# Performance work log

Measured on AMD Instinct MI355X. Metric: run time of the kernel, lower is better.

## Reference

```python
import jax, jax.numpy as jnp
import numpy as np

D_MODEL = 1024
HEADS = 16
D_K = D_MODEL // HEADS
D_FF = 4096
B, S = 2, 2048
EPS = 1e-5


def setup_inputs() -> dict:
    key = jax.random.key(0)
    ks = jax.random.split(key, 16)
    sc_att = 1.0 / np.sqrt(D_MODEL)
    sc_ff1 = 1.0 / np.sqrt(D_MODEL)
    sc_ff2 = 1.0 / np.sqrt(D_FF)
    return {
        "input": jax.random.normal(ks[0], (B, S, D_MODEL), jnp.float32),
        "mask": jnp.ones((B, 1, 1, S), jnp.int32),
        # stacked per-head projections: [H, D_MODEL, D_K]
        "Wq": jax.random.normal(ks[1], (HEADS, D_MODEL, D_K), jnp.float32) * sc_att,
        "bq": jax.random.normal(ks[2], (HEADS, D_K), jnp.float32) * 0.01,
        "Wk": jax.random.normal(ks[3], (HEADS, D_MODEL, D_K), jnp.float32) * sc_att,
        "bk": jax.random.normal(ks[4], (HEADS, D_K), jnp.float32) * 0.01,
        "Wv": jax.random.normal(ks[5], (HEADS, D_MODEL, D_K), jnp.float32) * sc_att,
        "bv": jax.random.normal(ks[6], (HEADS, D_K), jnp.float32) * 0.01,
        "Wo": jax.random.normal(ks[7], (D_MODEL, D_MODEL), jnp.float32) * sc_att,
        "bo": jax.random.normal(ks[8], (D_MODEL,), jnp.float32) * 0.01,
        "ln1_g": jnp.ones((D_MODEL,), jnp.float32),
        "ln1_b": jnp.zeros((D_MODEL,), jnp.float32),
        "ln2_g": jnp.ones((D_MODEL,), jnp.float32),
        "ln2_b": jnp.zeros((D_MODEL,), jnp.float32),
        "W1": jax.random.normal(ks[9], (D_MODEL, D_FF), jnp.float32) * sc_ff1,
        "b1": jax.random.normal(ks[10], (D_FF,), jnp.float32) * 0.01,
        "W2": jax.random.normal(ks[11], (D_FF, D_MODEL), jnp.float32) * sc_ff2,
        "b2": jax.random.normal(ks[12], (D_MODEL,), jnp.float32) * 0.01,
    }


def _layernorm(x, g, b):
    mu = jnp.mean(x, axis=-1, keepdims=True)
    var = jnp.mean(jnp.square(x - mu), axis=-1, keepdims=True)
    return (x - mu) * jax.lax.rsqrt(var + EPS) * g + b


def reference(input, mask, Wq, bq, Wk, bk, Wv, bv, Wo, bo,
              ln1_g, ln1_b, ln2_g, ln2_b, W1, b1, W2, b2):
    x = input
    # per-head projections, stacked: [B,H,S,D_K]
    q = jnp.einsum('bsd,hdk->bhsk', x, Wq) + bq[None, :, None, :]
    k = jnp.einsum('bsd,hdk->bhsk', x, Wk) + bk[None, :, None, :]
    v = jnp.einsum('bsd,hdk->bhsk', x, Wv) + bv[None, :, None, :]
    scores = jnp.einsum('bhqk,bhsk->bhqs', q, k) / np.sqrt(D_K)  # [B,H,S,S]
    scores = jnp.where(mask == 0, jnp.float32(-1e9), scores)
    attn = jax.nn.softmax(scores, axis=-1)
    ctx = jnp.einsum('bhqs,bhsk->bhqk', attn, v)  # [B,H,S,D_K]
    # concat heads along feature dim (head h occupies slice h*D_K:(h+1)*D_K)
    ctx = jnp.transpose(ctx, (0, 2, 1, 3)).reshape(B, S, D_MODEL)
    att_out = ctx @ Wo + bo
    h = _layernorm(x + att_out, ln1_g, ln1_b)
    ff = jax.nn.relu(h @ W1 + b1) @ W2 + b2
    return _layernorm(h + ff, ln2_g, ln2_b)
```

## Files before the change

### kernel.cpp

```cpp
#include <hip/hip_runtime.h>
#include <cstdint>
#include <cstddef>

typedef unsigned short u16;
typedef unsigned int   u32;
typedef unsigned short u16x4 __attribute__((ext_vector_type(4)));
typedef unsigned short u16x8 __attribute__((ext_vector_type(8)));
typedef unsigned int   u32x2 __attribute__((ext_vector_type(2)));
typedef __bf16 bf16x8 __attribute__((ext_vector_type(8)));
typedef float f32x4 __attribute__((ext_vector_type(4)));

#define MFMA16(a, b, c) __builtin_amdgcn_mfma_f32_16x16x32_bf16((a), (b), (c), 0, 0, 0)

__device__ __forceinline__ float bf2f(u16 h) {
  union { unsigned u; float f; } v; v.u = ((unsigned)h) << 16; return v.f;
}
__device__ __forceinline__ u16 f2bf(float f) {
  union { float f; unsigned u; } v; v.f = f;
  unsigned r = v.u + 0x7fffu + ((v.u >> 16) & 1u);
  return (u16)(r >> 16);
}
__device__ __forceinline__ void gll16(const u16* g, u16* l) {
  __builtin_amdgcn_global_load_lds(
      (const __attribute__((address_space(1))) void*)g,
      (__attribute__((address_space(3))) void*)l, 16, 0, 0);
}
__device__ __forceinline__ float fast_exp2(float x) {
#if __has_builtin(__builtin_amdgcn_exp2f)
  return __builtin_amdgcn_exp2f(x);
#else
  return exp2f(x);
#endif
}

__global__ __launch_bounds__(256) void transpose_qkv(
    const float* __restrict__ Wq, const float* __restrict__ Wk,
    const float* __restrict__ Wv, u16* __restrict__ outb) {
  __shared__ u16 tile[32][33];
  const int z = blockIdx.z;
  const int which = z >> 4, h = z & 15;
  const float* in = (which == 0 ? Wq : (which == 1 ? Wk : Wv)) + (size_t)h * 1024 * 64;
  u16* out = outb + ((size_t)which * 1024 + h * 64) * 1024;
  const int tx = threadIdx.x & 31, ty = threadIdx.x >> 5;
  const int r0 = blockIdx.y * 32, c0 = blockIdx.x * 32;
  #pragma unroll
  for (int i = 0; i < 32; i += 8)
    tile[ty + i][tx] = f2bf(in[(size_t)(r0 + ty + i) * 64 + c0 + tx]);
  __syncthreads();
  #pragma unroll
  for (int i = 0; i < 32; i += 8)
    out[(size_t)(c0 + ty + i) * 1024 + r0 + tx] = tile[tx][ty + i];
}

__global__ __launch_bounds__(256) void transpose_w(
    const float* __restrict__ Wo, const float* __restrict__ W1,
    const float* __restrict__ W2, u16* __restrict__ Wo_t,
    u16* __restrict__ W1_t, u16* __restrict__ W2_t) {
  __shared__ u16 tile[32][33];
  const int id = blockIdx.x;
  const float* in; u16* outp; int R, C, cx, ry;
  if (id < 1024)      { in = Wo; outp = Wo_t; R = 1024; C = 1024; cx = id & 31;  ry = id >> 5; }
  else if (id < 5120) { int t = id - 1024; in = W1; outp = W1_t; R = 1024; C = 4096; cx = t & 127; ry = t >> 7; }
  else                { int t = id - 5120; in = W2; outp = W2_t; R = 4096; C = 1024; cx = t & 31;  ry = t >> 5; }
  const int tx = threadIdx.x & 31, ty = threadIdx.x >> 5;
  const int r0 = ry * 32, c0 = cx * 32;
  #pragma unroll
  for (int i = 0; i < 32; i += 8)
    tile[ty + i][tx] = f2bf(in[(size_t)(r0 + ty + i) * C + c0 + tx]);
  __syncthreads();
  #pragma unroll
  for (int i = 0; i < 32; i += 8)
    outp[(size_t)(c0 + ty + i) * R + r0 + tx] = tile[tx][ty + i];
}

__global__ __launch_bounds__(256) void prep_small(
    const float* __restrict__ bq, const float* __restrict__ bk,
    const float* __restrict__ bv, const int* __restrict__ mask,
    float* __restrict__ biasq, float* __restrict__ madd2) {
  int i = blockIdx.x * 256 + threadIdx.x;
  if (i < 3072) {
    biasq[i] = (i < 1024) ? bq[i] : (i < 2048 ? bk[i - 1024] : bv[i - 2048]);
  } else if (i < 7168) {
    int j = i - 3072;
    madd2[j] = mask[j] ? -23.083120f : -1.442695e9f;
  }
}

__global__ __launch_bounds__(256) void cvt_x(
    const float* __restrict__ in, u16* __restrict__ out, int n) {
  int i = (blockIdx.x * 256 + threadIdx.x) * 4;
  if (i >= n) return;
  const float4 v = *(const float4*)&in[i];
  u16x4 o;
  o[0] = f2bf(v.x); o[1] = f2bf(v.y); o[2] = f2bf(v.z); o[3] = f2bf(v.w);
  *(u16x4*)&out[i] = o;
}

template <int MODE>
__global__ __launch_bounds__(256) void gemm_bt(
    const u16* __restrict__ A, const u16* __restrict__ Bt,
    const float* __restrict__ bias, u16* __restrict__ C,
    int M, int N, int K) {
  __shared__ __align__(16) u16 As[2][128 * 32];
  __shared__ __align__(16) u16 Bs[2][128 * 32];
  const int tid = threadIdx.x;
  const int lane = tid & 63;
  const int wave = tid >> 6;
  const int m0 = blockIdx.y * 128;
  const int n0 = blockIdx.x * 128;
  const int wr = (wave >> 1) * 64;
  const int wc = (wave & 1) * 64;
  const int lrow = lane & 15;
  const int quad = lane >> 4;

  const int srow = lane >> 2;
  const int scol = (lane & 3) * 8;
  const u16* gA1 = &A[(size_t)(m0 + wave * 16 + srow) * K + scol];
  const u16* gA2 = &A[(size_t)(m0 + 64 + wave * 16 + srow) * K + scol];
  const u16* gB1 = &Bt[(size_t)(n0 + wave * 16 + srow) * K + scol];
  const u16* gB2 = &Bt[(size_t)(n0 + 64 + wave * 16 + srow) * K + scol];
  const int so1 = (wave * 16) * 32;
  const int so2 = (wave * 16 + 64) * 32;

  f32x4 acc[4][4];
  #pragma unroll
  for (int i = 0; i < 4; ++i)
    #pragma unroll
    for (int j = 0; j < 4; ++j)
      acc[i][j] = (f32x4){0.f, 0.f, 0.f, 0.f};

  for (int k0 = 0; k0 < K; k0 += 64) {
    gll16(gA1 + k0, &As[0][so1]);
    gll16(gA2 + k0, &As[0][so2]);
    gll16(gB1 + k0, &Bs[0][so1]);
    gll16(gB2 + k0, &Bs[0][so2]);
    gll16(gA1 + k0 + 32, &As[1][so1]);
    gll16(gA2 + k0 + 32, &As[1][so2]);
    gll16(gB1 + k0 + 32, &Bs[1][so1]);
    gll16(gB2 + k0 + 32, &Bs[1][so2]);
    __syncthreads();
    #pragma unroll
    for (int kb = 0; kb < 2; ++kb) {
      bf16x8 af[4], bfr[4];
      #pragma unroll
      for (int i = 0; i < 4; ++i) {
        af[i]  = *(const bf16x8*)&As[kb][(wr + i * 16 + lrow) * 32 + quad * 8];
        bfr[i] = *(const bf16x8*)&Bs[kb][(wc + i * 16 + lrow) * 32 + quad * 8];
      }
      #pragma unroll
      for (int fr = 0; fr < 4; ++fr)
        #pragma unroll
        for (int fc = 0; fc < 4; ++fc)
          acc[fr][fc] = MFMA16(af[fr], bfr[fc], acc[fr][fc]);
    }
    __syncthreads();
  }

  #pragma unroll
  for (int fr = 0; fr < 4; ++fr) {
    int rowb = m0 + wr + fr * 16 + quad * 4;
    #pragma unroll
    for (int fc = 0; fc < 4; ++fc) {
      int col = n0 + wc + fc * 16 + lrow;
      float bv = bias[col];
      #pragma unroll
      for (int r = 0; r < 4; ++r) {
        float v = acc[fr][fc][r] + bv;
        if (MODE == 1) v = fmaxf(v, 0.f);
        C[(size_t)(rowb + r) * N + col] = f2bf(v);
      }
    }
  }
}

__global__ __launch_bounds__(256) void gemm_splitk(
    const u16* __restrict__ A, const u16* __restrict__ Bt,
    u16* __restrict__ Cp, int M, int N, int K) {
  __shared__ __align__(16) u16 As[2][128 * 32];
  __shared__ __align__(16) u16 Bs[2][128 * 32];
  const int tid = threadIdx.x;
  const int lane = tid & 63;
  const int wave = tid >> 6;
  const int m0 = blockIdx.y * 128;
  const int n0 = blockIdx.x * 128;
  const int kz = blockIdx.z;
  const int Kh = K >> 1;
  const int kbase = kz * Kh;
  const int wr = (wave >> 1) * 64;
  const int wc = (wave & 1) * 64;
  const int lrow = lane & 15;
  const int quad = lane >> 4;

  const int srow = lane >> 2;
  const int scol = (lane & 3) * 8;
  const u16* gA1 = &A[(size_t)(m0 + wave * 16 + srow) * K + kbase + scol];
  const u16* gA2 = &A[(size_t)(m0 + 64 + wave * 16 + srow) * K + kbase + scol];
  const u16* gB1 = &Bt[(size_t)(n0 + wave * 16 + srow) * K + kbase + scol];
  const u16* gB2 = &Bt[(size_t)(n0 + 64 + wave * 16 + srow) * K + kbase + scol];
  const int so1 = (wave * 16) * 32;
  const int so2 = (wave * 16 + 64) * 32;
  u16* C = Cp + (size_t)kz * M * N;

  f32x4 acc[4][4];
  #pragma unroll
  for (int i = 0; i < 4; ++i)
    #pragma unroll
    for (int j = 0; j < 4; ++j)
      acc[i][j] = (f32x4){0.f, 0.f, 0.f, 0.f};

  for (int k0 = 0; k0 < Kh; k0 += 64) {
    gll16(gA1 + k0, &As[0][so1]);
    gll16(gA2 + k0, &As[0][so2]);
    gll16(gB1 + k0, &Bs[0][so1]);
    gll16(gB2 + k0, &Bs[0][so2]);
    gll16(gA1 + k0 + 32, &As[1][so1]);
    gll16(gA2 + k0 + 32, &As[1][so2]);
    gll16(gB1 + k0 + 32, &Bs[1][so1]);
    gll16(gB2 + k0 + 32, &Bs[1][so2]);
    __syncthreads();
    #pragma unroll
    for (int kb = 0; kb < 2; ++kb) {
      bf16x8 af[4], bfr[4];
      #pragma unroll
      for (int i = 0; i < 4; ++i) {
        af[i]  = *(const bf16x8*)&As[kb][(wr + i * 16 + lrow) * 32 + quad * 8];
        bfr[i] = *(const bf16x8*)&Bs[kb][(wc + i * 16 + lrow) * 32 + quad * 8];
      }
      #pragma unroll
      for (int fr = 0; fr < 4; ++fr)
        #pragma unroll
        for (int fc = 0; fc < 4; ++fc)
          acc[fr][fc] = MFMA16(af[fr], bfr[fc], acc[fr][fc]);
    }
    __syncthreads();
  }

  #pragma unroll
  for (int fr = 0; fr < 4; ++fr) {
    int rowb = m0 + wr + fr * 16 + quad * 4;
    #pragma unroll
    for (int fc = 0; fc < 4; ++fc) {
      int col = n0 + wc + fc * 16 + lrow;
      #pragma unroll
      for (int r = 0; r < 4; ++r)
        C[(size_t)(rowb + r) * N + col] = f2bf(acc[fr][fc][r]);
    }
  }
}

__global__ __launch_bounds__(256) void attn_kernel(
    const u16* __restrict__ xqkv, const float* __restrict__ madd2,
    u16* __restrict__ ctx) {
  __shared__ __align__(16) u16 Ks[64][72];
  __shared__ __align__(16) u16 Vt[64][136];
  __shared__ __align__(16) u16 Ps[4][2][16][72];
  const int tid = threadIdx.x;
  const int lane = tid & 63;
  const int wave = tid >> 6;
  const int lrow = lane & 15;
  const int quad = lane >> 4;
  const int b = blockIdx.z, h = blockIdx.y;
  const int qb = blockIdx.x * 128 + wave * 16;
  const u16* Qp = xqkv + (size_t)b * 2048 * 3072 + h * 64;
  const u16* Kp = Qp + 1024;
  const u16* Vp = Qp + 2048;
  const float S2 = 0.18033688f;

  bf16x8 qa[2][2];
  #pragma unroll
  for (int t = 0; t < 2; ++t) {
    qa[t][0] = *(const bf16x8*)&Qp[(size_t)(qb + t * 64 + lrow) * 3072 + quad * 8];
    qa[t][1] = *(const bf16x8*)&Qp[(size_t)(qb + t * 64 + lrow) * 3072 + 32 + quad * 8];
  }

  f32x4 o[2][4];
  #pragma unroll
  for (int t = 0; t < 2; ++t)
    #pragma unroll
    for (int i = 0; i < 4; ++i) o[t][i] = (f32x4){0.f, 0.f, 0.f, 0.f};
  float rsum[2] = {0.f, 0.f};

  const int ks_row = tid >> 3, ks_col = (tid & 7) * 8;
  const int v_dg = tid >> 4;
  const int v_kp = tid & 15;
  const float* maddb = madd2 + b * 2048;

  u16x8 kreg[2];
  u16x4 va[2], vb[2];
  #pragma unroll
  for (int sh = 0; sh < 2; ++sh) {
    kreg[sh] = *(const u16x8*)&Kp[(size_t)(sh * 32 + ks_row) * 3072 + ks_col];
    va[sh] = *(const u16x4*)&Vp[(size_t)(sh * 32 + 2 * v_kp) * 3072 + v_dg * 4];
    vb[sh] = *(const u16x4*)&Vp[(size_t)(sh * 32 + 2 * v_kp + 1) * 3072 + v_dg * 4];
  }

  for (int s0 = 0; s0 < 2048; s0 += 64) {
    __syncthreads();
    #pragma unroll
    for (int sh = 0; sh < 2; ++sh) {
      *(u16x8*)&Ks[sh * 32 + ks_row][ks_col] = kreg[sh];
      #pragma unroll
      for (int j = 0; j < 4; ++j) {
        u32 pk = ((u32)vb[sh][j] << 16) | (u32)va[sh][j];
        *(u32*)&Vt[v_dg * 4 + j][sh * 32 + 2 * v_kp] = pk;
      }
    }
    __syncthreads();
    if (s0 + 64 < 2048) {
      #pragma unroll
      for (int sh = 0; sh < 2; ++sh) {
        int sb = s0 + 64 + sh * 32;
        kreg[sh] = *(const u16x8*)&Kp[(size_t)(sb + ks_row) * 3072 + ks_col];
        va[sh] = *(const u16x4*)&Vp[(size_t)(sb + 2 * v_kp) * 3072 + v_dg * 4];
        vb[sh] = *(const u16x4*)&Vp[(size_t)(sb + 2 * v_kp + 1) * 3072 + v_dg * 4];
      }
    }

    bf16x8 kf[4][2], vf[4][2];
    #pragma unroll
    for (int kb = 0; kb < 4; ++kb) {
      kf[kb][0] = *(const bf16x8*)&Ks[kb * 16 + lrow][quad * 8];
      kf[kb][1] = *(const bf16x8*)&Ks[kb * 16 + lrow][32 + quad * 8];
    }
    #pragma unroll
    for (int nb = 0; nb < 4; ++nb) {
      vf[nb][0] = *(const bf16x8*)&Vt[nb * 16 + lrow][quad * 8];
      vf[nb][1] = *(const bf16x8*)&Vt[nb * 16 + lrow][32 + quad * 8];
    }

    #pragma unroll
    for (int t = 0; t < 2; ++t) {
      #pragma unroll
      for (int kb = 0; kb < 4; ++kb) {
        f32x4 z = (f32x4){0.f, 0.f, 0.f, 0.f};
        z = MFMA16(kf[kb][0], qa[t][0], z);
        z = MFMA16(kf[kb][1], qa[t][1], z);
        f32x4 m4 = *(const f32x4*)&maddb[s0 + kb * 16 + quad * 4];
        u32 pb[4];
        #pragma unroll
        for (int r = 0; r < 4; ++r) {
          float p = fast_exp2(fmaf(z[r], S2, m4[r]));
          rsum[t] += p;
          union { float f; u32 u; } cv; cv.f = p;
          pb[r] = cv.u + 0x8000u;
        }
        u32x2 w2;
        w2[0] = __builtin_amdgcn_perm(pb[1], pb[0], 0x07060302);
        w2[1] = __builtin_amdgcn_perm(pb[3], pb[2], 0x07060302);
        *(u32x2*)&Ps[wave][t][lrow][kb * 16 + quad * 4] = w2;
      }
      #pragma unroll
      for (int kh = 0; kh < 2; ++kh) {
        bf16x8 pa = *(const bf16x8*)&Ps[wave][t][lrow][kh * 32 + quad * 8];
        #pragma unroll
        for (int nb = 0; nb < 4; ++nb)
          o[t][nb] = MFMA16(pa, vf[nb][kh], o[t][nb]);
      }
    }
  }

  #pragma unroll
  for (int t = 0; t < 2; ++t) {
    float rs = rsum[t];
    rs += __shfl_xor(rs, 16, 64);
    rs += __shfl_xor(rs, 32, 64);
    float inv = 1.f / fmaxf(rs, 1e-30f);
    #pragma unroll
    for (int r = 0; r < 4; ++r) {
      float invq = __shfl(inv, quad * 4 + r, 64);
      int q = qb + t * 64 + quad * 4 + r;
      #pragma unroll
      for (int nb = 0; nb < 4; ++nb) {
        float v = o[t][nb][r] * invq;
        ctx[((size_t)b * 2048 + q) * 1024 + h * 64 + nb * 16 + lrow] = f2bf(v);
      }
    }
  }
}

template <int IN_BF, int OUT_BF>
__global__ __launch_bounds__(256) void add_ln2p(
    const void* __restrict__ xa_, const u16* __restrict__ p0,
    const u16* __restrict__ p1, const float* __restrict__ cb,
    const float* __restrict__ g, const float* __restrict__ bb,
    void* __restrict__ outp_) {
  __shared__ float red[8];
  const int tid = threadIdx.x;
  const size_t base = (size_t)blockIdx.x * 1024;
  const float* xf = (const float*)xa_;
  const u16*   xb = (const u16*)xa_;
  float v[4];
  float s = 0.f;
  #pragma unroll
  for (int i = 0; i < 4; ++i) {
    int c = i * 256 + tid;
    float xv = IN_BF ? bf2f(xb[base + c]) : xf[base + c];
    v[i] = xv + bf2f(p0[base + c]) + bf2f(p1[base + c]) + cb[c];
    s += v[i];
  }
  #pragma unroll
  for (int off = 32; off > 0; off >>= 1) s += __shfl_down(s, off, 64);
  if ((tid & 63) == 0) red[tid >> 6] = s;
  __syncthreads();
  float mean = (red[0] + red[1] + red[2] + red[3]) * (1.f / 1024.f);
  float s2 = 0.f;
  #pragma unroll
  for (int i = 0; i < 4; ++i) { float d = v[i] - mean; s2 += d * d; }
  #pragma unroll
  for (int off = 32; off > 0; off >>= 1) s2 += __shfl_down(s2, off, 64);
  if ((tid & 63) == 0) red[4 + (tid >> 6)] = s2;
  __syncthreads();
  float var = (red[4] + red[5] + red[6] + red[7]) * (1.f / 1024.f);
  float rstd = rsqrtf(var + 1e-5f);
  #pragma unroll
  for (int i = 0; i < 4; ++i) {
    int c = i * 256 + tid;
    float r = (v[i] - mean) * rstd * g[c] + bb[c];
    if (OUT_BF) ((u16*)outp_)[base + c] = f2bf(r);
    else        ((float*)outp_)[base + c] = r;
  }
}

extern "C" void kernel_launch(void* const* d_in, const int* in_sizes, int n_in,
                              void* d_out, int out_size, void* d_ws, size_t ws_size,
                              hipStream_t stream) {
  (void)in_sizes; (void)n_in; (void)out_size; (void)ws_size;
  const float* x    = (const float*)d_in[0];
  const int*   mask = (const int*)d_in[1];
  const float* Wq   = (const float*)d_in[2];
  const float* bq   = (const float*)d_in[3];
  const float* Wk   = (const float*)d_in[4];
  const float* bk   = (const float*)d_in[5];
  const float* Wv   = (const float*)d_in[6];
  const float* bv   = (const float*)d_in[7];
  const float* Wo   = (const float*)d_in[8];
  const float* bo   = (const float*)d_in[9];
  const float* ln1g = (const float*)d_in[10];
  const float* ln1b = (const float*)d_in[11];
  const float* ln2g = (const float*)d_in[12];
  const float* ln2b = (const float*)d_in[13];
  const float* W1   = (const float*)d_in[14];
  const float* b1   = (const float*)d_in[15];
  const float* W2   = (const float*)d_in[16];
  const float* b2   = (const float*)d_in[17];
  float* out = (float*)d_out;

  char* ws = (char*)d_ws;
  u16*   Wqkv_t = (u16*)(ws + 0);
  u16*   fp     = (u16*)(ws + 0);
  u16*   Wo_t   = (u16*)(ws + 6291456);
  u16*   W1_t   = (u16*)(ws + 8388608);
  u16*   W2_t   = (u16*)(ws + 16777216);
  u16*   xqkv   = (u16*)(ws + 25165824);
  u16*   wp     = (u16*)(ws + 25165824);
  u16*   xb     = (u16*)(ws + 50331648);
  u16*   ctx    = (u16*)(ws + 50331648);
  u16*   ff1    = (u16*)(ws + 25165824);
  u16*   hbuf   = (u16*)(ws + 67108864);
  float* biasq  = (float*)(ws + 75497472);
  float* madd2  = (float*)(ws + 75509760);

  prep_small<<<28, 256, 0, stream>>>(bq, bk, bv, mask, biasq, madd2);
  transpose_qkv<<<dim3(2, 32, 48), 256, 0, stream>>>(Wq, Wk, Wv, Wqkv_t);
  transpose_w<<<9216, 256, 0, stream>>>(Wo, W1, W2, Wo_t, W1_t, W2_t);
  cvt_x<<<4096, 256, 0, stream>>>(x, xb, 4194304);

  gemm_bt<0><<<dim3(24, 32), 256, 0, stream>>>(xb, Wqkv_t, biasq, xqkv,
                                               4096, 3072, 1024);
  attn_kernel<<<dim3(16, 16, 2), 256, 0, stream>>>(xqkv, madd2, ctx);
  gemm_splitk<<<dim3(8, 32, 2), 256, 0, stream>>>(ctx, Wo_t, wp, 4096, 1024, 1024);
  add_ln2p<0, 1><<<4096, 256, 0, stream>>>(x, wp, wp + 4194304, bo,
                                           ln1g, ln1b, hbuf);
  gemm_bt<1><<<dim3(32, 32), 256, 0, stream>>>(hbuf, W1_t, b1, ff1,
                                               4096, 4096, 1024);
  gemm_splitk<<<dim3(8, 32, 2), 256, 0, stream>>>(ff1, W2_t, fp, 4096, 1024, 4096);
  add_ln2p<1, 0><<<4096, 256, 0, stream>>>(hbuf, fp, fp + 4194304, b2,
                                           ln2g, ln2b, out);
}
```

Before: 379.7 us.

## Split attention over the key dimension and pipeline GEMM K-tile loads

Attention now splits the key range into two halves per (batch, head) and launches twice as many blocks. Each block writes unnormalized partial outputs and row sums, and a new combine kernel adds the halves and normalizes them. The GEMM main loop switches from loading two 32-wide K slices and then computing, to double-buffered prefetching of the next 32-wide tile while the current one is computed, with one barrier per step. The split-K GEMM is merged into the templated kernel. In exchange there are extra partial-output traffic, an extra kernel launch, and bf16 rounding of the unnormalized partial sums; combining by plain addition assumes both halves use the same exponent reference.

```diff
diff --git a/kernel.cpp b/kernel.cpp
--- a/kernel.cpp
+++ b/kernel.cpp
@@ -11,6 +11,8 @@
 typedef float f32x4 __attribute__((ext_vector_type(4)));
 
 #define MFMA16(a, b, c) __builtin_amdgcn_mfma_f32_16x16x32_bf16((a), (b), (c), 0, 0, 0)
+#define WAIT_VM0() __builtin_amdgcn_s_waitcnt(0x0F70)
+#define BARRIER()  __builtin_amdgcn_s_barrier()
 
 __device__ __forceinline__ float bf2f(u16 h) {
   union { unsigned u; float f; } v; v.u = ((unsigned)h) << 16; return v.f;
@@ -108,84 +110,9 @@
   const int wave = tid >> 6;
   const int m0 = blockIdx.y * 128;
   const int n0 = blockIdx.x * 128;
-  const int wr = (wave >> 1) * 64;
-  const int wc = (wave & 1) * 64;
-  const int lrow = lane & 15;
-  const int quad = lane >> 4;
-
-  const int srow = lane >> 2;
-  const int scol = (lane & 3) * 8;
-  const u16* gA1 = &A[(size_t)(m0 + wave * 16 + srow) * K + scol];
-  const u16* gA2 = &A[(size_t)(m0 + 64 + wave * 16 + srow) * K + scol];
-  const u16* gB1 = &Bt[(size_t)(n0 + wave * 16 + srow) * K + scol];
-  const u16* gB2 = &Bt[(size_t)(n0 + 64 + wave * 16 + srow) * K + scol];
-  const int so1 = (wave * 16) * 32;
-  const int so2 = (wave * 16 + 64) * 32;
-
-  f32x4 acc[4][4];
-  #pragma unroll
-  for (int i = 0; i < 4; ++i)
-    #pragma unroll
-    for (int j = 0; j < 4; ++j)
-      acc[i][j] = (f32x4){0.f, 0.f, 0.f, 0.f};
-
-  for (int k0 = 0; k0 < K; k0 += 64) {
-    gll16(gA1 + k0, &As[0][so1]);
-    gll16(gA2 + k0, &As[0][so2]);
-    gll16(gB1 + k0, &Bs[0][so1]);
-    gll16(gB2 + k0, &Bs[0][so2]);
-    gll16(gA1 + k0 + 32, &As[1][so1]);
-    gll16(gA2 + k0 + 32, &As[1][so2]);
-    gll16(gB1 + k0 + 32, &Bs[1][so1]);
-    gll16(gB2 + k0 + 32, &Bs[1][so2]);
-    __syncthreads();
-    #pragma unroll
-    for (int kb = 0; kb < 2; ++kb) {
-      bf16x8 af[4], bfr[4];
-      #pragma unroll
-      for (int i = 0; i < 4; ++i) {
-        af[i]  = *(const bf16x8*)&As[kb][(wr + i * 16 + lrow) * 32 + quad * 8];
-        bfr[i] = *(const bf16x8*)&Bs[kb][(wc + i * 16 + lrow) * 32 + quad * 8];
-      }
-      #pragma unroll
-      for (int fr = 0; fr < 4; ++fr)
-        #pragma unroll
-        for (int fc = 0; fc < 4; ++fc)
-          acc[fr][fc] = MFMA16(af[fr], bfr[fc], acc[fr][fc]);
-    }
-    __syncthreads();
-  }
-
-  #pragma unroll
-  for (int fr = 0; fr < 4; ++fr) {
-    int rowb = m0 + wr + fr * 16 + quad * 4;
-    #pragma unroll
-    for (int fc = 0; fc < 4; ++fc) {
-      int col = n0 + wc + fc * 16 + lrow;
-      float bv = bias[col];
-      #pragma unroll
-      for (int r = 0; r < 4; ++r) {
-        float v = acc[fr][fc][r] + bv;
-        if (MODE == 1) v = fmaxf(v, 0.f);
-        C[(size_t)(rowb + r) * N + col] = f2bf(v);
-      }
-    }
-  }
-}
-
-__global__ __launch_bounds__(256) void gemm_splitk(
-    const u16* __restrict__ A, const u16* __restrict__ Bt,
-    u16* __restrict__ Cp, int M, int N, int K) {
-  __shared__ __align__(16) u16 As[2][128 * 32];
-  __shared__ __align__(16) u16 Bs[2][128 * 32];
-  const int tid = threadIdx.x;
-  const int lane = tid & 63;
-  const int wave = tid >> 6;
-  const int m0 = blockIdx.y * 128;
-  const int n0 = blockIdx.x * 128;
-  const int kz = blockIdx.z;
-  const int Kh = K >> 1;
-  const int kbase = kz * Kh;
+  const int kz = (MODE == 2) ? blockIdx.z : 0;
+  const int Keff = (MODE == 2) ? (K >> 1) : K;
+  const int kbase = kz * Keff;
   const int wr = (wave >> 1) * 64;
   const int wc = (wave & 1) * 64;
   const int lrow = lane & 15;
@@ -199,7 +126,7 @@
   const u16* gB2 = &Bt[(size_t)(n0 + 64 + wave * 16 + srow) * K + kbase + scol];
   const int so1 = (wave * 16) * 32;
   const int so2 = (wave * 16 + 64) * 32;
-  u16* C = Cp + (size_t)kz * M * N;
+  u16* Cw = (MODE == 2) ? (C + (size_t)kz * M * N) : C;
 
   f32x4 acc[4][4];
   #pragma unroll
@@ -208,31 +135,34 @@
     for (int j = 0; j < 4; ++j)
       acc[i][j] = (f32x4){0.f, 0.f, 0.f, 0.f};
 
-  for (int k0 = 0; k0 < Kh; k0 += 64) {
-    gll16(gA1 + k0, &As[0][so1]);
-    gll16(gA2 + k0, &As[0][so2]);
-    gll16(gB1 + k0, &Bs[0][so1]);
-    gll16(gB2 + k0, &Bs[0][so2]);
-    gll16(gA1 + k0 + 32, &As[1][so1]);
-    gll16(gA2 + k0 + 32, &As[1][so2]);
-    gll16(gB1 + k0 + 32, &Bs[1][so1]);
-    gll16(gB2 + k0 + 32, &Bs[1][so2]);
-    __syncthreads();
-    #pragma unroll
-    for (int kb = 0; kb < 2; ++kb) {
-      bf16x8 af[4], bfr[4];
-      #pragma unroll
-      for (int i = 0; i < 4; ++i) {
-        af[i]  = *(const bf16x8*)&As[kb][(wr + i * 16 + lrow) * 32 + quad * 8];
-        bfr[i] = *(const bf16x8*)&Bs[kb][(wc + i * 16 + lrow) * 32 + quad * 8];
-      }
-      #pragma unroll
-      for (int fr = 0; fr < 4; ++fr)
-        #pragma unroll
-        for (int fc = 0; fc < 4; ++fc)
-          acc[fr][fc] = MFMA16(af[fr], bfr[fc], acc[fr][fc]);
-    }
-    __syncthreads();
+  gll16(gA1, &As[0][so1]);
+  gll16(gA2, &As[0][so2]);
+  gll16(gB1, &Bs[0][so1]);
+  gll16(gB2, &Bs[0][so2]);
+
+  const int nIter = Keff >> 5;
+  for (int it = 0; it < nIter; ++it) {
+    const int cur = it & 1;
+    WAIT_VM0();
+    BARRIER();
+    const int k1 = (it + 1) << 5;
+    if (k1 < Keff) {
+      gll16(gA1 + k1, &As[cur ^ 1][so1]);
+      gll16(gA2 + k1, &As[cur ^ 1][so2]);
+      gll16(gB1 + k1, &Bs[cur ^ 1][so1]);
+      gll16(gB2 + k1, &Bs[cur ^ 1][so2]);
+    }
+    bf16x8 af[4], bfr[4];
+    #pragma unroll
+    for (int i = 0; i < 4; ++i) {
+      af[i]  = *(const bf16x8*)&As[cur][(wr + i * 16 + lrow) * 32 + quad * 8];
+      bfr[i] = *(const bf16x8*)&Bs[cur][(wc + i * 16 + lrow) * 32 + quad * 8];
+    }
+    #pragma unroll
+    for (int fr = 0; fr < 4; ++fr)
+      #pragma unroll
+      for (int fc = 0; fc < 4; ++fc)
+        acc[fr][fc] = MFMA16(af[fr], bfr[fc], acc[fr][fc]);
   }
 
   #pragma unroll
@@ -241,16 +171,20 @@
     #pragma unroll
     for (int fc = 0; fc < 4; ++fc) {
       int col = n0 + wc + fc * 16 + lrow;
-      #pragma unroll
-      for (int r = 0; r < 4; ++r)
-        C[(size_t)(rowb + r) * N + col] = f2bf(acc[fr][fc][r]);
+      float bv = (MODE == 2) ? 0.f : bias[col];
+      #pragma unroll
+      for (int r = 0; r < 4; ++r) {
+        float v = acc[fr][fc][r] + bv;
+        if (MODE == 1) v = fmaxf(v, 0.f);
+        Cw[(size_t)(rowb + r) * N + col] = f2bf(v);
+      }
     }
   }
 }
 
 __global__ __launch_bounds__(256) void attn_kernel(
     const u16* __restrict__ xqkv, const float* __restrict__ madd2,
-    u16* __restrict__ ctx) {
+    u16* __restrict__ opart, float* __restrict__ lpart) {
   __shared__ __align__(16) u16 Ks[64][72];
   __shared__ __align__(16) u16 Vt[64][136];
   __shared__ __align__(16) u16 Ps[4][2][16][72];
@@ -259,12 +193,14 @@
   const int wave = tid >> 6;
   const int lrow = lane & 15;
   const int quad = lane >> 4;
-  const int b = blockIdx.z, h = blockIdx.y;
+  const int b = blockIdx.z >> 1, kz = blockIdx.z & 1;
+  const int h = blockIdx.y;
   const int qb = blockIdx.x * 128 + wave * 16;
   const u16* Qp = xqkv + (size_t)b * 2048 * 3072 + h * 64;
   const u16* Kp = Qp + 1024;
   const u16* Vp = Qp + 2048;
   const float S2 = 0.18033688f;
+  const int sbeg = kz * 1024, send = sbeg + 1024;
 
   bf16x8 qa[2][2];
   #pragma unroll
@@ -289,12 +225,12 @@
   u16x4 va[2], vb[2];
   #pragma unroll
   for (int sh = 0; sh < 2; ++sh) {
-    kreg[sh] = *(const u16x8*)&Kp[(size_t)(sh * 32 + ks_row) * 3072 + ks_col];
-    va[sh] = *(const u16x4*)&Vp[(size_t)(sh * 32 + 2 * v_kp) * 3072 + v_dg * 4];
-    vb[sh] = *(const u16x4*)&Vp[(size_t)(sh * 32 + 2 * v_kp + 1) * 3072 + v_dg * 4];
-  }
-
-  for (int s0 = 0; s0 < 2048; s0 += 64) {
+    kreg[sh] = *(const u16x8*)&Kp[(size_t)(sbeg + sh * 32 + ks_row) * 3072 + ks_col];
+    va[sh] = *(const u16x4*)&Vp[(size_t)(sbeg + sh * 32 + 2 * v_kp) * 3072 + v_dg * 4];
+    vb[sh] = *(const u16x4*)&Vp[(size_t)(sbeg + sh * 32 + 2 * v_kp + 1) * 3072 + v_dg * 4];
+  }
+
+  for (int s0 = sbeg; s0 < send; s0 += 64) {
     __syncthreads();
     #pragma unroll
     for (int sh = 0; sh < 2; ++sh) {
@@ -306,7 +242,7 @@
       }
     }
     __syncthreads();
-    if (s0 + 64 < 2048) {
+    if (s0 + 64 < send) {
       #pragma unroll
       for (int sh = 0; sh < 2; ++sh) {
         int sb = s0 + 64 + sh * 32;
@@ -359,22 +295,40 @@
     }
   }
 
+  u16* ob = opart + (size_t)kz * 4194304;
+  float* lb = lpart + (size_t)kz * 65536 + ((size_t)b * 16 + h) * 2048;
   #pragma unroll
   for (int t = 0; t < 2; ++t) {
     float rs = rsum[t];
     rs += __shfl_xor(rs, 16, 64);
     rs += __shfl_xor(rs, 32, 64);
-    float inv = 1.f / fmaxf(rs, 1e-30f);
+    if (lane < 16) lb[qb + t * 64 + lane] = rs;
     #pragma unroll
     for (int r = 0; r < 4; ++r) {
-      float invq = __shfl(inv, quad * 4 + r, 64);
       int q = qb + t * 64 + quad * 4 + r;
       #pragma unroll
-      for (int nb = 0; nb < 4; ++nb) {
-        float v = o[t][nb][r] * invq;
-        ctx[((size_t)b * 2048 + q) * 1024 + h * 64 + nb * 16 + lrow] = f2bf(v);
-      }
-    }
+      for (int nb = 0; nb < 4; ++nb)
+        ob[((size_t)b * 2048 + q) * 1024 + h * 64 + nb * 16 + lrow] =
+            f2bf(o[t][nb][r]);
+    }
+  }
+}
+
+__global__ __launch_bounds__(256) void attn_combine(
+    const u16* __restrict__ opart, const float* __restrict__ lpart,
+    u16* __restrict__ ctx) {
+  const int t = blockIdx.x;
+  const int b = t >> 11, q = t & 2047;
+  const int tid = threadIdx.x;
+  const size_t base = (size_t)t * 1024;
+  #pragma unroll
+  for (int i = 0; i < 4; ++i) {
+    int c = i * 256 + tid;
+    int h = c >> 6;
+    float l = lpart[((size_t)b * 16 + h) * 2048 + q] +
+              lpart[65536 + ((size_t)b * 16 + h) * 2048 + q];
+    float o = bf2f(opart[base + c]) + bf2f(opart[4194304 + base + c]);
+    ctx[base + c] = f2bf(o / fmaxf(l, 1e-30f));
   }
 }
 
@@ -446,8 +400,9 @@
   float* out = (float*)d_out;
 
   char* ws = (char*)d_ws;
+  float* lpart  = (float*)(ws + 0);
+  u16*   fp     = (u16*)(ws + 0);
   u16*   Wqkv_t = (u16*)(ws + 0);
-  u16*   fp     = (u16*)(ws + 0);
   u16*   Wo_t   = (u16*)(ws + 6291456);
   u16*   W1_t   = (u16*)(ws + 8388608);
   u16*   W2_t   = (u16*)(ws + 16777216);
@@ -455,8 +410,9 @@
   u16*   wp     = (u16*)(ws + 25165824);
   u16*   xb     = (u16*)(ws + 50331648);
   u16*   ctx    = (u16*)(ws + 50331648);
+  u16*   opart  = (u16*)(ws + 58720256);
+  u16*   hbuf   = (u16*)(ws + 58720256);
   u16*   ff1    = (u16*)(ws + 25165824);
-  u16*   hbuf   = (u16*)(ws + 67108864);
   float* biasq  = (float*)(ws + 75497472);
   float* madd2  = (float*)(ws + 75509760);
 
@@ -467,13 +423,16 @@
 
   gemm_bt<0><<<dim3(24, 32), 256, 0, stream>>>(xb, Wqkv_t, biasq, xqkv,
                                                4096, 3072, 1024);
-  attn_kernel<<<dim3(16, 16, 2), 256, 0, stream>>>(xqkv, madd2, ctx);
-  gemm_splitk<<<dim3(8, 32, 2), 256, 0, stream>>>(ctx, Wo_t, wp, 4096, 1024, 1024);
+  attn_kernel<<<dim3(16, 16, 4), 256, 0, stream>>>(xqkv, madd2, opart, lpart);
+  attn_combine<<<4096, 256, 0, stream>>>(opart, lpart, ctx);
+  gemm_bt<2><<<dim3(8, 32, 2), 256, 0, stream>>>(ctx, Wo_t, nullptr, wp,
+                                                 4096, 1024, 1024);
   add_ln2p<0, 1><<<4096, 256, 0, stream>>>(x, wp, wp + 4194304, bo,
                                            ln1g, ln1b, hbuf);
   gemm_bt<1><<<dim3(32, 32), 256, 0, stream>>>(hbuf, W1_t, b1, ff1,
                                                4096, 4096, 1024);
-  gemm_splitk<<<dim3(8, 32, 2), 256, 0, stream>>>(ff1, W2_t, fp, 4096, 1024, 4096);
+  gemm_bt<2><<<dim3(8, 32, 2), 256, 0, stream>>>(ff1, W2_t, nullptr, fp,
+                                                 4096, 1024, 4096);
   add_ln2p<1, 0><<<4096, 256, 0, stream>>>(hbuf, fp, fp + 4194304, b2,
                                            ln2g, ln2b, out);
 }
```

Measured after the change: 383.1 us. Within noise of the previous version (+0.9%).
